# Performance work log

Measured on AMD Instinct MI355X. Metric: run time of the kernel, lower is better.

Reference implementation:

```python
import jax, jax.numpy as jnp
import numpy as np


def setup_inputs() -> dict:
    key = jax.random.key(0)
    k1, k2, k3, k4 = jax.random.split(key, 4)
    T = 64            # decoder_batch_len (target steps)
    B = 32            # batch_size
    V = 50257         # decoder vocab size
    L = 400           # encoder (source) length
    rows = T * B
    vocab_ds = jax.random.uniform(k1, (rows, V), dtype=jnp.float32)
    attns = jax.random.uniform(k2, (rows, L), dtype=jnp.float32)
    p_gens = jax.random.uniform(k3, (rows, 1), dtype=jnp.float32)
    sources = jax.random.randint(k4, (L, B), 0, V, dtype=jnp.int64)
    return {
        "vocab_ds": vocab_ds,
        "attns": attns,
        "p_gens": p_gens,
        "sources": sources,
        "decoder_batch_len": T,
    }


def reference(vocab_ds, attns, p_gens, sources, decoder_batch_len):
    # vocab_ds: (T*B, V), attns: (T*B, L), p_gens: (T*B, 1), sources: (L, B)
    rows, V = vocab_ds.shape
    vocab_dists = p_gens * vocab_ds                      # gated generation dist
    attn_dists = (1.0 - p_gens) * attns                  # gated copy dist
    # sources.T tiled over decoder steps -> per-row vocab ids, shape (T*B, L)
    sources_rep = jnp.tile(sources.T, (decoder_batch_len, 1))
    row_idx = jnp.arange(rows)[:, None]                  # (T*B, 1) broadcasts over L
    # torch scatter_ (overwrite semantics) of copy probs into vocab slots
    attn_dists_projected = jnp.zeros((rows, V), dtype=vocab_ds.dtype).at[
        row_idx, sources_rep
    ].set(attn_dists, mode="drop")
    final_dists = attn_dists_projected + vocab_dists
    return final_dists
```

## Files before the change

kernel.cpp:

```cpp
#include <hip/hip_runtime.h>

typedef float f32x4 __attribute__((ext_vector_type(4)));

#define LMAX 1024

__global__ __launch_bounds__(256) void mask_kernel(
    const int* __restrict__ sources, int* __restrict__ vlast, int L, int B)
{
    const int b = blockIdx.x;
    __shared__ int s_col[LMAX];
    const bool use_lds = (L <= LMAX);
    if (use_lds) {
        for (int l = threadIdx.x; l < L; l += blockDim.x)
            s_col[l] = sources[(size_t)l * B + b];
    }
    __syncthreads();
    for (int l = threadIdx.x; l < L; l += blockDim.x) {
        const int v = use_lds ? s_col[l] : sources[(size_t)l * B + b];
        int keep = v;
        if (use_lds) {
            for (int l2 = l + 1; l2 < L; ++l2)
                if (s_col[l2] == v) { keep = -1; break; }
        } else {
            for (int l2 = l + 1; l2 < L; ++l2)
                if (sources[(size_t)l2 * B + b] == v) { keep = -1; break; }
        }
        vlast[(size_t)l * B + b] = keep;
    }
}

__global__ __launch_bounds__(256) void scale_kernel(
    const float* __restrict__ vd, const float* __restrict__ pgs,
    float* __restrict__ out, int V, int CPR)
{
    const int bid   = blockIdx.x;
    const int row   = bid / CPR;
    const int chunk = bid - row * CPR;
    const int tid   = threadIdx.x;
    const size_t base = (size_t)row * (size_t)V;
    const float pg = pgs[row];

    const int mis  = (int)(base & 3);
    const int pre  = mis ? (4 - mis) : 0;
    const int preN = pre < V ? pre : V;
    const int nvec = (V - preN) >> 2;
    const int per  = (nvec + CPR - 1) / CPR;
    const int v0   = chunk * per;
    const int v1   = (v0 + per < nvec) ? (v0 + per) : nvec;

    const f32x4* __restrict__ v4 = (const f32x4*)(vd + base + preN);
    f32x4* __restrict__ o4       = (f32x4*)(out + base + preN);
    for (int i = v0 + tid; i < v1; i += 256) {
        f32x4 x = v4[i];
        x *= pg;
        o4[i] = x;
    }
    if (chunk == 0)
        for (int j = tid; j < preN; j += 256)
            out[base + j] = pg * vd[base + j];
    if (chunk == CPR - 1)
        for (int j = preN + (nvec << 2) + tid; j < V; j += 256)
            out[base + j] = pg * vd[base + j];
}

__global__ __launch_bounds__(256) void scatter_kernel(
    const float* __restrict__ vd, const float* __restrict__ attns,
    const float* __restrict__ pgs, const int* __restrict__ vlast,
    float* __restrict__ out, int V, int L, int B)
{
    const int row = blockIdx.x;
    const int b = row % B;
    const float pg = pgs[row];
    const float gate = 1.0f - pg;
    const size_t base = (size_t)row * (size_t)V;
    for (int l = threadIdx.x; l < L; l += 256) {
        const int v = vlast[(size_t)l * B + b];
        if (v >= 0 && v < V)
            out[base + v] = fmaf(pg, vd[base + v],
                                 gate * attns[(size_t)row * L + l]);
    }
}

__global__ __launch_bounds__(256) void fused_fallback_kernel(
    const float* __restrict__ vocab_ds, const float* __restrict__ attns,
    const float* __restrict__ p_gens, const int* __restrict__ sources,
    float* __restrict__ out, int V, int L, int B)
{
    const int row = blockIdx.x;
    const int tid = threadIdx.x;
    const size_t base = (size_t)row * (size_t)V;
    const float pg = p_gens[row];

    const int mis  = (int)(base & 3);
    const int pre  = mis ? (4 - mis) : 0;
    const int preN = pre < V ? pre : V;
    for (int j = tid; j < preN; j += blockDim.x)
        out[base + j] = pg * vocab_ds[base + j];
    const int nvec = (V - preN) >> 2;
    const f32x4* __restrict__ v4 = (const f32x4*)(vocab_ds + base + preN);
    f32x4* __restrict__ o4       = (f32x4*)(out + base + preN);
    for (int i = tid; i < nvec; i += blockDim.x) {
        f32x4 x = v4[i];
        x *= pg;
        o4[i] = x;
    }
    for (int j = preN + (nvec << 2) + tid; j < V; j += blockDim.x)
        out[base + j] = pg * vocab_ds[base + j];

    __shared__ int s_src[512];
    const int b = row % B;
    const bool use_lds = (L <= 512);
    if (use_lds) {
        for (int l = tid; l < L; l += blockDim.x)
            s_src[l] = sources[(size_t)l * B + b];
    }
    __syncthreads();
    const float gate = 1.0f - pg;
    for (int l = tid; l < L; l += blockDim.x) {
        const int v = use_lds ? s_src[l] : sources[(size_t)l * B + b];
        if (v < 0 || v >= V) continue;
        bool last = true;
        for (int l2 = l + 1; l2 < L; ++l2) {
            const int v2 = use_lds ? s_src[l2] : sources[(size_t)l2 * B + b];
            if (v2 == v) { last = false; break; }
        }
        if (last) {
            const float a = gate * attns[(size_t)row * L + l];
            out[base + v] = pg * vocab_ds[base + v] + a;
        }
    }
}

extern "C" void kernel_launch(void* const* d_in, const int* in_sizes, int n_in,
                              void* d_out, int out_size, void* d_ws, size_t ws_size,
                              hipStream_t stream) {
    const float* vocab_ds = (const float*)d_in[0];
    const float* attns    = (const float*)d_in[1];
    const float* p_gens   = (const float*)d_in[2];
    const int*   sources  = (const int*)d_in[3];
    const int rows = in_sizes[2];
    const int V    = in_sizes[0] / rows;
    const int L    = in_sizes[1] / rows;
    const int B    = in_sizes[3] / L;
    float* out = (float*)d_out;

    const size_t mask_bytes = (size_t)L * (size_t)B * sizeof(int);
    if (ws_size >= mask_bytes) {
        int* vlast = (int*)d_ws;
        const int CPR = 8;
        mask_kernel<<<B, 256, 0, stream>>>(sources, vlast, L, B);
        scale_kernel<<<rows * CPR, 256, 0, stream>>>(vocab_ds, p_gens, out, V, CPR);
        scatter_kernel<<<rows, 256, 0, stream>>>(vocab_ds, attns, p_gens,
                                                 vlast, out, V, L, B);
    } else {
        fused_fallback_kernel<<<rows, 256, 0, stream>>>(
            vocab_ds, attns, p_gens, sources, out, V, L, B);
    }
}
```

Before: 269.8 us.

## Fuse scale and scatter via per-row LDS bitmap and sorted source lookup

Replaces the separate scale and scatter kernels with one kernel per row. Each source column is sorted by vocab id (last occurrence wins through the stable rank), an LDS bitmap marks the copied slots, and each vectorized element gets its copy term through a binary search before a single nontemporal store. This removes the second pass that reread and rewrote scattered output, and drops the 8-chunk-per-row split to one block per row. The cost is bitmap setup and LDS traffic per row, plus less parallelism per row since only 2048 blocks launch.

```diff
diff --git a/kernel.cpp b/kernel.cpp
--- a/kernel.cpp
+++ b/kernel.cpp
@@ -1,83 +1,121 @@
 #include <hip/hip_runtime.h>
 
 typedef float f32x4 __attribute__((ext_vector_type(4)));
+typedef unsigned int uint32;
 
-#define LMAX 1024
+#define MAXV 51200
+#define NWMAX (MAXV / 32 + 1)
+#define LPAD 1024
 
-__global__ __launch_bounds__(256) void mask_kernel(
-    const int* __restrict__ sources, int* __restrict__ vlast, int L, int B)
+__global__ __launch_bounds__(256) void sort_kernel(
+    const int* __restrict__ sources, int* __restrict__ sv, int* __restrict__ sl,
+    int L, int B, int V)
 {
     const int b = blockIdx.x;
-    __shared__ int s_col[LMAX];
-    const bool use_lds = (L <= LMAX);
-    if (use_lds) {
-        for (int l = threadIdx.x; l < L; l += blockDim.x)
-            s_col[l] = sources[(size_t)l * B + b];
+    __shared__ int s_col[LPAD];
+    for (int l = threadIdx.x; l < L; l += 256) {
+        const int v = sources[(size_t)l * B + b];
+        s_col[l] = (v >= 0 && v < V) ? v : 0x7FFFFFFF;
     }
     __syncthreads();
-    for (int l = threadIdx.x; l < L; l += blockDim.x) {
-        const int v = use_lds ? s_col[l] : sources[(size_t)l * B + b];
-        int keep = v;
-        if (use_lds) {
-            for (int l2 = l + 1; l2 < L; ++l2)
-                if (s_col[l2] == v) { keep = -1; break; }
-        } else {
-            for (int l2 = l + 1; l2 < L; ++l2)
-                if (sources[(size_t)l2 * B + b] == v) { keep = -1; break; }
+    int* __restrict__ svb = sv + (size_t)b * L;
+    int* __restrict__ slb = sl + (size_t)b * L;
+    for (int l = threadIdx.x; l < L; l += 256) {
+        const int v = s_col[l];
+        int rank = 0;
+        for (int k = 0; k < L; ++k) {
+            const int vk = s_col[k];
+            rank += (vk < v) || (vk == v && k < l);
         }
-        vlast[(size_t)l * B + b] = keep;
+        svb[rank] = v;
+        slb[rank] = l;
     }
 }
 
-__global__ __launch_bounds__(256) void scale_kernel(
-    const float* __restrict__ vd, const float* __restrict__ pgs,
-    float* __restrict__ out, int V, int CPR)
+__global__ __launch_bounds__(256) void fused_kernel(
+    const float* __restrict__ vd, const float* __restrict__ attns,
+    const float* __restrict__ pgs, const int* __restrict__ sv,
+    const int* __restrict__ sl, float* __restrict__ out, int V, int L, int B)
 {
-    const int bid   = blockIdx.x;
-    const int row   = bid / CPR;
-    const int chunk = bid - row * CPR;
-    const int tid   = threadIdx.x;
+    const int row = blockIdx.x;
+    const int tid = threadIdx.x;
+    const int b   = row % B;
+
+    __shared__ uint32 bm[NWMAX];
+    __shared__ int    s_v[LPAD];
+    __shared__ int    s_l[LPAD];
+    __shared__ float  s_attn[LPAD];
+
+    const int NW = (V + 31) >> 5;
+    for (int w = tid; w < NW + 1; w += 256) bm[w] = 0u;
+    const int* __restrict__ svb = sv + (size_t)b * L;
+    const int* __restrict__ slb = sl + (size_t)b * L;
+    for (int t = tid; t < LPAD; t += 256) {
+        s_v[t]    = (t < L) ? svb[t] : 0x7FFFFFFF;
+        s_l[t]    = (t < L) ? slb[t] : 0;
+        s_attn[t] = (t < L) ? attns[(size_t)row * L + t] : 0.0f;
+    }
+    __syncthreads();
+    for (int t = tid; t < L; t += 256) {
+        const int v = s_v[t];
+        if (v < V) atomicOr(&bm[v >> 5], 1u << (v & 31));
+    }
+    __syncthreads();
+
+    const float pg   = pgs[row];
+    const float gate = 1.0f - pg;
     const size_t base = (size_t)row * (size_t)V;
-    const float pg = pgs[row];
+
+    auto lookup = [&](int j) -> float {
+        int lo = 0, hi = LPAD;
+        while (lo < hi) {
+            const int mid = (lo + hi) >> 1;
+            if (s_v[mid] <= j) lo = mid + 1; else hi = mid;
+        }
+        return gate * s_attn[s_l[lo - 1]];
+    };
 
     const int mis  = (int)(base & 3);
     const int pre  = mis ? (4 - mis) : 0;
     const int preN = pre < V ? pre : V;
+    if (tid < preN) {
+        const int j = tid;
+        float x = pg * vd[base + j];
+        if ((bm[j >> 5] >> (j & 31)) & 1u) x += lookup(j);
+        __builtin_nontemporal_store(x, &out[base + j]);
+    }
+
     const int nvec = (V - preN) >> 2;
-    const int per  = (nvec + CPR - 1) / CPR;
-    const int v0   = chunk * per;
-    const int v1   = (v0 + per < nvec) ? (v0 + per) : nvec;
-
     const f32x4* __restrict__ v4 = (const f32x4*)(vd + base + preN);
     f32x4* __restrict__ o4       = (f32x4*)(out + base + preN);
-    for (int i = v0 + tid; i < v1; i += 256) {
+
+    auto proc = [&](int i) {
         f32x4 x = v4[i];
         x *= pg;
-        o4[i] = x;
+        const int j0 = preN + (i << 2);
+        const int w  = j0 >> 5;
+        const uint32 sh = (uint32)(j0 & 31);
+        uint32 bits;
+        if (sh <= 28u) bits = (bm[w] >> sh) & 0xFu;
+        else           bits = ((bm[w] >> sh) | (bm[w + 1] << (32u - sh))) & 0xFu;
+        if (bits) {
+#pragma unroll
+            for (int e = 0; e < 4; ++e)
+                if ((bits >> e) & 1u) x[e] += lookup(j0 + e);
+        }
+        __builtin_nontemporal_store(x, &o4[i]);
+    };
+
+    int i = tid;
+    for (; i + 768 < nvec; i += 1024) {
+        proc(i); proc(i + 256); proc(i + 512); proc(i + 768);
     }
-    if (chunk == 0)
-        for (int j = tid; j < preN; j += 256)
-            out[base + j] = pg * vd[base + j];
-    if (chunk == CPR - 1)
-        for (int j = preN + (nvec << 2) + tid; j < V; j += 256)
-            out[base + j] = pg * vd[base + j];
-}
+    for (; i < nvec; i += 256) proc(i);
 
-__global__ __launch_bounds__(256) void scatter_kernel(
-    const float* __restrict__ vd, const float* __restrict__ attns,
-    const float* __restrict__ pgs, const int* __restrict__ vlast,
-    float* __restrict__ out, int V, int L, int B)
-{
-    const int row = blockIdx.x;
-    const int b = row % B;
-    const float pg = pgs[row];
-    const float gate = 1.0f - pg;
-    const size_t base = (size_t)row * (size_t)V;
-    for (int l = threadIdx.x; l < L; l += 256) {
-        const int v = vlast[(size_t)l * B + b];
-        if (v >= 0 && v < V)
-            out[base + v] = fmaf(pg, vd[base + v],
-                                 gate * attns[(size_t)row * L + l]);
+    for (int j = preN + (nvec << 2) + tid; j < V; j += 256) {
+        float x = pg * vd[base + j];
+        if ((bm[j >> 5] >> (j & 31)) & 1u) x += lookup(j);
+        __builtin_nontemporal_store(x, &out[base + j]);
     }
 }
 
@@ -144,14 +182,14 @@
     const int B    = in_sizes[3] / L;
     float* out = (float*)d_out;
 
-    const size_t mask_bytes = (size_t)L * (size_t)B * sizeof(int);
-    if (ws_size >= mask_bytes) {
-        int* vlast = (int*)d_ws;
-        const int CPR = 8;
-        mask_kernel<<<B, 256, 0, stream>>>(sources, vlast, L, B);
-        scale_kernel<<<rows * CPR, 256, 0, stream>>>(vocab_ds, p_gens, out, V, CPR);
-        scatter_kernel<<<rows, 256, 0, stream>>>(vocab_ds, attns, p_gens,
-                                                 vlast, out, V, L, B);
+    const size_t need = (size_t)B * (size_t)L * 2 * sizeof(int);
+    const bool fits = (ws_size >= need) && (V <= (NWMAX - 1) * 32) && (L <= LPAD);
+    if (fits) {
+        int* sv = (int*)d_ws;
+        int* sl = sv + (size_t)B * (size_t)L;
+        sort_kernel<<<B, 256, 0, stream>>>(sources, sv, sl, L, B, V);
+        fused_kernel<<<rows, 256, 0, stream>>>(vocab_ds, attns, p_gens,
+                                               sv, sl, out, V, L, B);
     } else {
         fused_fallback_kernel<<<rows, 256, 0, stream>>>(
             vocab_ds, attns, p_gens, sources, out, V, L, B);
```

Measured after the change: 234.4 us. 1.15x faster.
